# Kernel optimization log

Hardware: AMD Instinct MI355X
Metric: run time of the kernel (lower is better)

## Reference

```python
import jax, jax.numpy as jnp
import numpy as np

D_MODEL = 1024
NUM_HEADS = 16
D_K = D_MODEL // NUM_HEADS


def setup_inputs() -> dict:
    key = jax.random.key(0)
    ks = jax.random.split(key, 12)
    B, S = 2, 2048
    s = 1.0 / np.sqrt(D_MODEL)
    return {
        "Q": jax.random.normal(ks[0], (B, S, D_MODEL), jnp.float32),
        "K": jax.random.normal(ks[1], (B, S, D_MODEL), jnp.float32),
        "V": jax.random.normal(ks[2], (B, S, D_MODEL), jnp.float32),
        "Wq": jax.random.normal(ks[3], (D_MODEL, D_MODEL), jnp.float32) * s,
        "bq": jax.random.normal(ks[4], (D_MODEL,), jnp.float32) * s,
        "Wk": jax.random.normal(ks[5], (D_MODEL, D_MODEL), jnp.float32) * s,
        "bk": jax.random.normal(ks[6], (D_MODEL,), jnp.float32) * s,
        "Wv": jax.random.normal(ks[7], (D_MODEL, D_MODEL), jnp.float32) * s,
        "bv": jax.random.normal(ks[8], (D_MODEL,), jnp.float32) * s,
        "Wfc": jax.random.normal(ks[9], (D_MODEL, D_MODEL), jnp.float32) * s,
        "bfc": jax.random.normal(ks[10], (D_MODEL,), jnp.float32) * s,
    }


def reference(Q, K, V, Wq, bq, Wk, bk, Wv, bv, Wfc, bfc):
    B, S, _ = Q.shape
    # Linear projections, then split heads: [B, S, D] -> [B, H, S, d_k]
    def split_heads(x):
        return x.reshape(B, S, NUM_HEADS, D_K).transpose(0, 2, 1, 3)
    q = split_heads(Q @ Wq + bq)
    k = split_heads(K @ Wk + bk)
    v = split_heads(V @ Wv + bv)
    # Scaled dot-product attention (mask=None path)
    scores = jnp.einsum('bhqd,bhkd->bhqk', q, k) / jnp.sqrt(jnp.asarray(D_K, q.dtype))
    attention = jax.nn.softmax(scores, axis=-1)  # [B, H, S, S]
    context = jnp.einsum('bhqk,bhkd->bhqd', attention, v)
    context = context.transpose(0, 2, 1, 3).reshape(B, S, D_MODEL)
    output = context @ Wfc + bfc
    return output, attention
```

## Files before the change

### kernel.cpp

```cpp
#include <hip/hip_runtime.h>
#include <hip/hip_bf16.h>
#include <stdint.h>


typedef __bf16 bf16_t;
typedef __bf16 bf16x8 __attribute__((ext_vector_type(8)));
typedef float  f32x4  __attribute__((ext_vector_type(4)));

#define MFMA16(a, b, c) __builtin_amdgcn_mfma_f32_16x16x32_bf16((a), (b), (c), 0, 0, 0)

__global__ __launch_bounds__(256)
void wtrans_kernel(const float* w0, const float* w1, const float* w2,
                   const float* w3, bf16_t* wt)
{
  const float* W = blockIdx.z == 0 ? w0 : blockIdx.z == 1 ? w1
                 : blockIdx.z == 2 ? w2 : w3;
  bf16_t* O = wt + ((size_t)blockIdx.z << 20);
  __shared__ bf16_t tile[64][72];
  const int t = threadIdx.x;
  const int r0 = blockIdx.y * 64, c0 = blockIdx.x * 64;
  {
    const int r = t >> 2, cg = (t & 3) * 16;
    const float4* src = (const float4*)(W + (size_t)(r0 + r) * 1024 + c0 + cg);
#pragma unroll
    for (int u = 0; u < 4; ++u) {
      float4 f = src[u];
      tile[r][cg + u * 4 + 0] = (bf16_t)f.x;
      tile[r][cg + u * 4 + 1] = (bf16_t)f.y;
      tile[r][cg + u * 4 + 2] = (bf16_t)f.z;
      tile[r][cg + u * 4 + 3] = (bf16_t)f.w;
    }
  }
  __syncthreads();
  {
    const int c = t >> 2, rg = (t & 3) * 16;
    bf16x8 v0, v1;
#pragma unroll
    for (int u = 0; u < 8; ++u) { v0[u] = tile[rg + u][c]; v1[u] = tile[rg + 8 + u][c]; }
    bf16x8* dst = (bf16x8*)(O + (size_t)(c0 + c) * 1024 + r0 + rg);
    dst[0] = v0; dst[1] = v1;
  }
}

__global__ __launch_bounds__(256)
void vtrans_kernel(const bf16_t* vb, bf16_t* vT)
{
  __shared__ bf16_t tile[64][72];
  const int t = threadIdx.x;
  const int bh = blockIdx.y;
  const int s0 = blockIdx.x * 64;
  {
    const int s = t >> 2, dg = (t & 3) * 16;
    const bf16x8* src = (const bf16x8*)(vb + ((size_t)bh * 2048 + s0 + s) * 64 + dg);
    bf16x8 a = src[0], b = src[1];
#pragma unroll
    for (int u = 0; u < 8; ++u) { tile[s][dg + u] = a[u]; tile[s][dg + 8 + u] = b[u]; }
  }
  __syncthreads();
  {
    const int d = t >> 2, sg = (t & 3) * 16;
    bf16x8 v0, v1;
#pragma unroll
    for (int u = 0; u < 8; ++u) { v0[u] = tile[sg + u][d]; v1[u] = tile[sg + 8 + u][d]; }
    bf16x8* dst = (bf16x8*)(vT + ((size_t)bh * 64 + d) * 2048 + s0 + sg);
    dst[0] = v0; dst[1] = v1;
  }
}

template<bool A_BF16, bool OUT_SPLIT>
__global__ __launch_bounds__(256, 2)
void gemm_kernel(const void* A0, const void* A1, const void* A2,
                 const bf16_t* WTbase,
                 const float* b0, const float* b1, const float* b2,
                 void* Obase, size_t ostride)
{
  const int z = blockIdx.z;
  const void*  Aptr = z == 0 ? A0 : z == 1 ? A1 : A2;
  const float* bias = z == 0 ? b0 : z == 1 ? b1 : b2;
  const bf16_t* WT  = WTbase + ((size_t)z << 20);

  __shared__ bf16_t As[128 * 32];
  __shared__ bf16_t Bs[128 * 32];

  const int tid = threadIdx.x;
  const int lane = tid & 63, wv = tid >> 6;
  const int quad = lane >> 4, lr = lane & 15;
  const int wm = wv >> 1, wn = wv & 1;
  const int lin2 = blockIdx.y * 8 + blockIdx.x;
  const int idx  = lin2 >> 3;
  const int m0 = (((lin2 & 7) << 2) + (idx >> 3)) * 128;
  const int n0 = (idx & 7) * 128;

  f32x4 acc[4][4];
#pragma unroll
  for (int i = 0; i < 4; ++i)
#pragma unroll
    for (int j = 0; j < 4; ++j) acc[i][j] = (f32x4){0.f, 0.f, 0.f, 0.f};

  const int srow = tid >> 1;
  const int shalf = tid & 1;
  const int swz = (srow >> 1) & 3;
  bf16_t* as0 = &As[srow * 32 + (((shalf * 2)    ) ^ swz) * 8];
  bf16_t* as1 = &As[srow * 32 + (((shalf * 2) + 1) ^ swz) * 8];
  bf16_t* bs0 = &Bs[srow * 32 + (((shalf * 2)    ) ^ swz) * 8];
  bf16_t* bs1 = &Bs[srow * 32 + (((shalf * 2) + 1) ^ swz) * 8];

  for (int kt = 0; kt < 1024; kt += 32) {
    bf16x8 av0, av1, bv0, bv1;
    if (A_BF16) {
      const bf16x8* p = (const bf16x8*)((const bf16_t*)Aptr +
                          (size_t)(m0 + srow) * 1024 + kt + shalf * 16);
      av0 = p[0]; av1 = p[1];
    } else {
      const float4* p = (const float4*)((const float*)Aptr +
                          (size_t)(m0 + srow) * 1024 + kt + shalf * 16);
      float4 f0 = p[0], f1 = p[1], f2 = p[2], f3 = p[3];
      av0[0]=(bf16_t)f0.x; av0[1]=(bf16_t)f0.y; av0[2]=(bf16_t)f0.z; av0[3]=(bf16_t)f0.w;
      av0[4]=(bf16_t)f1.x; av0[5]=(bf16_t)f1.y; av0[6]=(bf16_t)f1.z; av0[7]=(bf16_t)f1.w;
      av1[0]=(bf16_t)f2.x; av1[1]=(bf16_t)f2.y; av1[2]=(bf16_t)f2.z; av1[3]=(bf16_t)f2.w;
      av1[4]=(bf16_t)f3.x; av1[5]=(bf16_t)f3.y; av1[6]=(bf16_t)f3.z; av1[7]=(bf16_t)f3.w;
    }
    {
      const bf16x8* p = (const bf16x8*)(WT + (size_t)(n0 + srow) * 1024 + kt + shalf * 16);
      bv0 = p[0]; bv1 = p[1];
    }
    __syncthreads();
    *(bf16x8*)as0 = av0; *(bf16x8*)as1 = av1;
    *(bf16x8*)bs0 = bv0; *(bf16x8*)bs1 = bv1;
    __syncthreads();
    bf16x8 af[4], bfr[4];
#pragma unroll
    for (int i = 0; i < 4; ++i) {
      const int row = wm * 64 + i * 16 + lr;
      af[i] = *(bf16x8*)&As[row * 32 + (quad ^ ((row >> 1) & 3)) * 8];
      const int nn = wn * 64 + i * 16 + lr;
      bfr[i] = *(bf16x8*)&Bs[nn * 32 + (quad ^ ((nn >> 1) & 3)) * 8];
    }
#pragma unroll
    for (int i = 0; i < 4; ++i)
#pragma unroll
      for (int j = 0; j < 4; ++j)
        acc[i][j] = MFMA16(af[i], bfr[j], acc[i][j]);
  }

  if (OUT_SPLIT) {
    bf16_t* O = (bf16_t*)Obase + (size_t)z * ostride;
#pragma unroll
    for (int i = 0; i < 4; ++i) {
      const int mbase = m0 + wm * 64 + i * 16 + quad * 4;
#pragma unroll
      for (int j = 0; j < 4; ++j) {
        const int n = n0 + wn * 64 + j * 16 + lr;
        const float bv = bias[n];
        const int h = n >> 6, d = n & 63;
#pragma unroll
        for (int r = 0; r < 4; ++r) {
          const int m = mbase + r;
          const int b = m >> 11, s = m & 2047;
          O[((size_t)(b * 16 + h) * 2048 + s) * 64 + d] = (bf16_t)(acc[i][j][r] + bv);
        }
      }
    }
  } else {
    float* O = (float*)Obase;
#pragma unroll
    for (int i = 0; i < 4; ++i) {
      const int mbase = m0 + wm * 64 + i * 16 + quad * 4;
#pragma unroll
      for (int j = 0; j < 4; ++j) {
        const int n = n0 + wn * 64 + j * 16 + lr;
        const float bv = bias[n];
#pragma unroll
        for (int r = 0; r < 4; ++r)
          O[(size_t)(mbase + r) * 1024 + n] = acc[i][j][r] + bv;
      }
    }
  }
}

__global__ __launch_bounds__(256, 2)
void attn_kernel(const bf16_t* qb, const bf16_t* kb, const bf16_t* vT,
                 float* attn, bf16_t* ctx)
{
  __shared__ bf16_t P[16 * 2048];
  __shared__ float wpart[4][16];
  __shared__ float inv16[16];
  const int tid = threadIdx.x;
  const int lane = tid & 63, wv = tid >> 6;
  const int quad = lane >> 4, lr = lane & 15;
  const int lin  = blockIdx.y * 128 + blockIdx.x;
  const int virt = ((lin & 7) << 9) + (lin >> 3);
  const int bh   = virt >> 7;
  const int row0 = (virt & 127) * 16;

  const bf16x8* qp = (const bf16x8*)(qb + ((size_t)bh * 2048 + row0 + lr) * 64 + quad * 8);
  const bf16x8 a0 = qp[0];
  const bf16x8 a1 = qp[4];

  float sums[4] = {0.f, 0.f, 0.f, 0.f};

  for (int ct = 0; ct < 32; ++ct) {
    const int n0 = wv * 512 + ct * 16;
    const bf16x8* kp = (const bf16x8*)(kb + ((size_t)bh * 2048 + n0 + lr) * 64 + quad * 8);
    const bf16x8 b0v = kp[0];
    const bf16x8 b1v = kp[4];
    f32x4 sacc = {0.f, 0.f, 0.f, 0.f};
    sacc = MFMA16(a0, b0v, sacc);
    sacc = MFMA16(a1, b1v, sacc);
#pragma unroll
    for (int r = 0; r < 4; ++r) {
      const float p = __expf(sacc[r] * 0.125f);
      const bf16_t pb = (bf16_t)p;
      sums[r] += (float)pb;
      const int prow = quad * 4 + r;
      P[prow * 2048 + ((n0 + lr) ^ ((prow & 7) << 3))] = pb;
    }
  }
#pragma unroll
  for (int m = 1; m < 16; m <<= 1) {
#pragma unroll
    for (int r = 0; r < 4; ++r) sums[r] += __shfl_xor(sums[r], m, 64);
  }
  if (lr == 0) {
#pragma unroll
    for (int r = 0; r < 4; ++r) wpart[wv][quad * 4 + r] = sums[r];
  }
  __syncthreads();
  if (tid < 16)
    inv16[tid] = 1.0f / (wpart[0][tid] + wpart[1][tid] + wpart[2][tid] + wpart[3][tid]);
  __syncthreads();

  {
    float* abase = attn + ((size_t)bh * 2048 + row0) * 2048 + tid * 8;
    for (int r = 0; r < 16; ++r) {
      const float inv = inv16[r];
      const bf16x8 pv = *(const bf16x8*)&P[r * 2048 + ((tid * 8) ^ ((r & 7) << 3))];
      f32x4 o0, o1;
      o0[0] = (float)pv[0] * inv; o0[1] = (float)pv[1] * inv;
      o0[2] = (float)pv[2] * inv; o0[3] = (float)pv[3] * inv;
      o1[0] = (float)pv[4] * inv; o1[1] = (float)pv[5] * inv;
      o1[2] = (float)pv[6] * inv; o1[3] = (float)pv[7] * inv;
      f32x4* dst = (f32x4*)(abase + (size_t)r * 2048);
      __builtin_nontemporal_store(o0, dst);
      __builtin_nontemporal_store(o1, dst + 1);
    }
  }

  {
    f32x4 cacc = {0.f, 0.f, 0.f, 0.f};
    const bf16_t* vbase = vT + ((size_t)bh * 64 + wv * 16 + lr) * 2048;
    for (int kt = 0; kt < 64; ++kt) {
      const bf16x8 af  = *(const bf16x8*)&P[lr * 2048 + ((kt * 32 + quad * 8) ^ ((lr & 7) << 3))];
      const bf16x8 bfv = *(const bf16x8*)(vbase + kt * 32 + quad * 8);
      cacc = MFMA16(af, bfv, cacc);
    }
    const int b = bh >> 4, h = bh & 15;
#pragma unroll
    for (int r = 0; r < 4; ++r) {
      const int row = quad * 4 + r;
      ctx[(size_t)(b * 2048 + row0 + row) * 1024 + h * 64 + wv * 16 + lr] =
          (bf16_t)(cacc[r] * inv16[row]);
    }
  }
}

extern "C" void kernel_launch(void* const* d_in, const int* in_sizes, int n_in,
                              void* d_out, int out_size, void* d_ws, size_t ws_size,
                              hipStream_t stream)
{
  const float* Q   = (const float*)d_in[0];
  const float* K   = (const float*)d_in[1];
  const float* V   = (const float*)d_in[2];
  const float* Wq  = (const float*)d_in[3];
  const float* bq  = (const float*)d_in[4];
  const float* Wk  = (const float*)d_in[5];
  const float* bk  = (const float*)d_in[6];
  const float* Wv  = (const float*)d_in[7];
  const float* bv  = (const float*)d_in[8];
  const float* Wfc = (const float*)d_in[9];
  const float* bfc = (const float*)d_in[10];

  char* ws = (char*)d_ws;
  bf16_t* wt   = (bf16_t*)ws;
  bf16_t* qb   = (bf16_t*)(ws + (size_t)8  * (1 << 20));
  bf16_t* kb   = (bf16_t*)(ws + (size_t)16 * (1 << 20));
  bf16_t* vb   = (bf16_t*)(ws + (size_t)24 * (1 << 20));
  bf16_t* vT   = (bf16_t*)(ws + (size_t)32 * (1 << 20));
  bf16_t* ctx  = (bf16_t*)(ws + (size_t)40 * (1 << 20));

  float* out  = (float*)d_out;
  float* attn = out + (size_t)4194304;

  dim3 blk(256);
  wtrans_kernel<<<dim3(16, 16, 4), blk, 0, stream>>>(Wq, Wk, Wv, Wfc, wt);
  gemm_kernel<false, true><<<dim3(8, 32, 3), blk, 0, stream>>>(
      Q, K, V, wt, bq, bk, bv, qb, (size_t)4194304);
  vtrans_kernel<<<dim3(32, 32), blk, 0, stream>>>(vb, vT);
  attn_kernel<<<dim3(128, 32), blk, 0, stream>>>(qb, kb, vT, attn, ctx);
  gemm_kernel<true, false><<<dim3(8, 32, 1), blk, 0, stream>>>(
      ctx, ctx, ctx, wt + ((size_t)3 << 20), bfc, bfc, bfc, out, 0);
}
```

Baseline: 884.5 us.

## Double-buffer GEMM with direct global-to-LDS loads and fuse V transpose into projection

Rewrites the projection GEMM main loop to use a 64-wide K tile with double-buffered LDS. The weight tile (and the A tile when it is already bf16) is fetched with global_load_lds, so the load for the next tile overlaps the MFMAs on the current one and the loop has one barrier per step. The V projection now writes its output directly in transposed [b,h,d,s] layout, which removes the separate vtrans kernel and its round trip through memory. LDS use grows to 64KB per block, which may reduce occupancy at the requested 2 blocks per CU.

After: 907.3 us. +2.6%, slower.

```diff
diff --git a/kernel.cpp b/kernel.cpp
--- a/kernel.cpp
+++ b/kernel.cpp
@@ -5,9 +5,14 @@
 
 typedef __bf16 bf16_t;
 typedef __bf16 bf16x8 __attribute__((ext_vector_type(8)));
+typedef __bf16 bf16x4 __attribute__((ext_vector_type(4)));
 typedef float  f32x4  __attribute__((ext_vector_type(4)));
 
 #define MFMA16(a, b, c) __builtin_amdgcn_mfma_f32_16x16x32_bf16((a), (b), (c), 0, 0, 0)
+
+#define GLDS(g, l) __builtin_amdgcn_global_load_lds( \
+    (const __attribute__((address_space(1))) void*)(g), \
+    (__attribute__((address_space(3))) void*)(l), 16, 0, 0)
 
 __global__ __launch_bounds__(256)
 void wtrans_kernel(const float* w0, const float* w1, const float* w2,
@@ -42,45 +47,20 @@
   }
 }
 
-__global__ __launch_bounds__(256)
-void vtrans_kernel(const bf16_t* vb, bf16_t* vT)
-{
-  __shared__ bf16_t tile[64][72];
-  const int t = threadIdx.x;
-  const int bh = blockIdx.y;
-  const int s0 = blockIdx.x * 64;
-  {
-    const int s = t >> 2, dg = (t & 3) * 16;
-    const bf16x8* src = (const bf16x8*)(vb + ((size_t)bh * 2048 + s0 + s) * 64 + dg);
-    bf16x8 a = src[0], b = src[1];
-#pragma unroll
-    for (int u = 0; u < 8; ++u) { tile[s][dg + u] = a[u]; tile[s][dg + 8 + u] = b[u]; }
-  }
-  __syncthreads();
-  {
-    const int d = t >> 2, sg = (t & 3) * 16;
-    bf16x8 v0, v1;
-#pragma unroll
-    for (int u = 0; u < 8; ++u) { v0[u] = tile[sg + u][d]; v1[u] = tile[sg + 8 + u][d]; }
-    bf16x8* dst = (bf16x8*)(vT + ((size_t)bh * 64 + d) * 2048 + s0 + sg);
-    dst[0] = v0; dst[1] = v1;
-  }
-}
-
 template<bool A_BF16, bool OUT_SPLIT>
 __global__ __launch_bounds__(256, 2)
 void gemm_kernel(const void* A0, const void* A1, const void* A2,
                  const bf16_t* WTbase,
                  const float* b0, const float* b1, const float* b2,
-                 void* Obase, size_t ostride)
+                 void* Obase, size_t ostride, bf16_t* vTout)
 {
   const int z = blockIdx.z;
   const void*  Aptr = z == 0 ? A0 : z == 1 ? A1 : A2;
   const float* bias = z == 0 ? b0 : z == 1 ? b1 : b2;
   const bf16_t* WT  = WTbase + ((size_t)z << 20);
 
-  __shared__ bf16_t As[128 * 32];
-  __shared__ bf16_t Bs[128 * 32];
+  __shared__ bf16_t As[2][128 * 64];
+  __shared__ bf16_t Bs[2][128 * 64];
 
   const int tid = threadIdx.x;
   const int lane = tid & 63, wv = tid >> 6;
@@ -97,67 +77,137 @@
 #pragma unroll
     for (int j = 0; j < 4; ++j) acc[i][j] = (f32x4){0.f, 0.f, 0.f, 0.f};
 
-  const int srow = tid >> 1;
-  const int shalf = tid & 1;
-  const int swz = (srow >> 1) & 3;
-  bf16_t* as0 = &As[srow * 32 + (((shalf * 2)    ) ^ swz) * 8];
-  bf16_t* as1 = &As[srow * 32 + (((shalf * 2) + 1) ^ swz) * 8];
-  bf16_t* bs0 = &Bs[srow * 32 + (((shalf * 2)    ) ^ swz) * 8];
-  bf16_t* bs1 = &Bs[srow * 32 + (((shalf * 2) + 1) ^ swz) * 8];
-
-  for (int kt = 0; kt < 1024; kt += 32) {
-    bf16x8 av0, av1, bv0, bv1;
+  const int gr = wv * 8 + (lane >> 3);
+  const int gc = ((lane & 7) ^ (lane >> 3)) << 3;
+  const bf16_t* bsrc = WT + (size_t)(n0 + gr) * 1024 + gc;
+  const bf16_t* absrc = (const bf16_t*)Aptr + (size_t)(m0 + gr) * 1024 + gc;
+
+  const int ar_ = tid >> 1, ah_ = tid & 1;
+  const float* afsrc = (const float*)Aptr + (size_t)(m0 + ar_) * 1024 + ah_ * 32;
+  int awofs[4];
+#pragma unroll
+  for (int c = 0; c < 4; ++c)
+    awofs[c] = ar_ * 64 + ((((ah_ << 2) + c) ^ (ar_ & 7)) << 3);
+
+  int arow[4], brow[4];
+#pragma unroll
+  for (int i = 0; i < 4; ++i) {
+    arow[i] = (wm * 64 + i * 16 + lr) * 64;
+    brow[i] = (wn * 64 + i * 16 + lr) * 64;
+  }
+  const int ach0 = ((quad)     ^ (lr & 7)) << 3;
+  const int ach1 = ((4 + quad) ^ (lr & 7)) << 3;
+
+  {
     if (A_BF16) {
-      const bf16x8* p = (const bf16x8*)((const bf16_t*)Aptr +
-                          (size_t)(m0 + srow) * 1024 + kt + shalf * 16);
-      av0 = p[0]; av1 = p[1];
+#pragma unroll
+      for (int n = 0; n < 4; ++n)
+        GLDS(absrc + n * 32768, &As[0][(n * 32 + wv * 8) * 64]);
     } else {
-      const float4* p = (const float4*)((const float*)Aptr +
-                          (size_t)(m0 + srow) * 1024 + kt + shalf * 16);
-      float4 f0 = p[0], f1 = p[1], f2 = p[2], f3 = p[3];
-      av0[0]=(bf16_t)f0.x; av0[1]=(bf16_t)f0.y; av0[2]=(bf16_t)f0.z; av0[3]=(bf16_t)f0.w;
-      av0[4]=(bf16_t)f1.x; av0[5]=(bf16_t)f1.y; av0[6]=(bf16_t)f1.z; av0[7]=(bf16_t)f1.w;
-      av1[0]=(bf16_t)f2.x; av1[1]=(bf16_t)f2.y; av1[2]=(bf16_t)f2.z; av1[3]=(bf16_t)f2.w;
-      av1[4]=(bf16_t)f3.x; av1[5]=(bf16_t)f3.y; av1[6]=(bf16_t)f3.z; av1[7]=(bf16_t)f3.w;
-    }
-    {
-      const bf16x8* p = (const bf16x8*)(WT + (size_t)(n0 + srow) * 1024 + kt + shalf * 16);
-      bv0 = p[0]; bv1 = p[1];
+      const float4* p = (const float4*)afsrc;
+      float4 areg[8];
+#pragma unroll
+      for (int u = 0; u < 8; ++u) areg[u] = p[u];
+#pragma unroll
+      for (int n = 0; n < 4; ++n)
+        GLDS(bsrc + n * 32768, &Bs[0][(n * 32 + wv * 8) * 64]);
+#pragma unroll
+      for (int c = 0; c < 4; ++c) {
+        const float4 f0 = areg[2 * c], f1 = areg[2 * c + 1];
+        bf16x8 v;
+        v[0]=(bf16_t)f0.x; v[1]=(bf16_t)f0.y; v[2]=(bf16_t)f0.z; v[3]=(bf16_t)f0.w;
+        v[4]=(bf16_t)f1.x; v[5]=(bf16_t)f1.y; v[6]=(bf16_t)f1.z; v[7]=(bf16_t)f1.w;
+        *(bf16x8*)&As[0][awofs[c]] = v;
+      }
+    }
+    if (A_BF16) {
+#pragma unroll
+      for (int n = 0; n < 4; ++n)
+        GLDS(bsrc + n * 32768, &Bs[0][(n * 32 + wv * 8) * 64]);
     }
     __syncthreads();
-    *(bf16x8*)as0 = av0; *(bf16x8*)as1 = av1;
-    *(bf16x8*)bs0 = bv0; *(bf16x8*)bs1 = bv1;
-    __syncthreads();
-    bf16x8 af[4], bfr[4];
-#pragma unroll
-    for (int i = 0; i < 4; ++i) {
-      const int row = wm * 64 + i * 16 + lr;
-      af[i] = *(bf16x8*)&As[row * 32 + (quad ^ ((row >> 1) & 3)) * 8];
-      const int nn = wn * 64 + i * 16 + lr;
-      bfr[i] = *(bf16x8*)&Bs[nn * 32 + (quad ^ ((nn >> 1) & 3)) * 8];
-    }
-#pragma unroll
-    for (int i = 0; i < 4; ++i)
-#pragma unroll
-      for (int j = 0; j < 4; ++j)
-        acc[i][j] = MFMA16(af[i], bfr[j], acc[i][j]);
+  }
+
+  for (int t = 0; t < 16; ++t) {
+    const int cur = t & 1, nxt = cur ^ 1;
+    const int ktn = t * 64 + 64;
+    float4 areg[8];
+    if (t < 15) {
+      if (A_BF16) {
+#pragma unroll
+        for (int n = 0; n < 4; ++n)
+          GLDS(absrc + n * 32768 + ktn, &As[nxt][(n * 32 + wv * 8) * 64]);
+      } else {
+        const float4* p = (const float4*)(afsrc + ktn);
+#pragma unroll
+        for (int u = 0; u < 8; ++u) areg[u] = p[u];
+      }
+#pragma unroll
+      for (int n = 0; n < 4; ++n)
+        GLDS(bsrc + n * 32768 + ktn, &Bs[nxt][(n * 32 + wv * 8) * 64]);
+    }
+#pragma unroll
+    for (int h = 0; h < 2; ++h) {
+      const int ach = h ? ach1 : ach0;
+      bf16x8 af[4], bfv[4];
+#pragma unroll
+      for (int i = 0; i < 4; ++i) af[i]  = *(const bf16x8*)&As[cur][arow[i] + ach];
+#pragma unroll
+      for (int j = 0; j < 4; ++j) bfv[j] = *(const bf16x8*)&Bs[cur][brow[j] + ach];
+#pragma unroll
+      for (int i = 0; i < 4; ++i)
+#pragma unroll
+        for (int j = 0; j < 4; ++j)
+          acc[i][j] = MFMA16(af[i], bfv[j], acc[i][j]);
+    }
+    if (t < 15) {
+      if (!A_BF16) {
+#pragma unroll
+        for (int c = 0; c < 4; ++c) {
+          const float4 f0 = areg[2 * c], f1 = areg[2 * c + 1];
+          bf16x8 v;
+          v[0]=(bf16_t)f0.x; v[1]=(bf16_t)f0.y; v[2]=(bf16_t)f0.z; v[3]=(bf16_t)f0.w;
+          v[4]=(bf16_t)f1.x; v[5]=(bf16_t)f1.y; v[6]=(bf16_t)f1.z; v[7]=(bf16_t)f1.w;
+          *(bf16x8*)&As[nxt][awofs[c]] = v;
+        }
+      }
+      __syncthreads();
+    }
   }
 
   if (OUT_SPLIT) {
-    bf16_t* O = (bf16_t*)Obase + (size_t)z * ostride;
-#pragma unroll
-    for (int i = 0; i < 4; ++i) {
-      const int mbase = m0 + wm * 64 + i * 16 + quad * 4;
-#pragma unroll
-      for (int j = 0; j < 4; ++j) {
-        const int n = n0 + wn * 64 + j * 16 + lr;
-        const float bv = bias[n];
-        const int h = n >> 6, d = n & 63;
-#pragma unroll
-        for (int r = 0; r < 4; ++r) {
-          const int m = mbase + r;
-          const int b = m >> 11, s = m & 2047;
-          O[((size_t)(b * 16 + h) * 2048 + s) * 64 + d] = (bf16_t)(acc[i][j][r] + bv);
+    if (z == 2) {
+#pragma unroll
+      for (int i = 0; i < 4; ++i) {
+        const int mbase = m0 + wm * 64 + i * 16 + quad * 4;
+        const int bb = mbase >> 11, s0 = mbase & 2047;
+#pragma unroll
+        for (int j = 0; j < 4; ++j) {
+          const int n = n0 + wn * 64 + j * 16 + lr;
+          const float bv = bias[n];
+          const int h = n >> 6, d = n & 63;
+          bf16x4 vv;
+#pragma unroll
+          for (int r = 0; r < 4; ++r) vv[r] = (bf16_t)(acc[i][j][r] + bv);
+          *(bf16x4*)&vTout[((size_t)((bb * 16 + h) * 64 + d)) * 2048 + s0] = vv;
+        }
+      }
+    } else {
+      bf16_t* O = (bf16_t*)Obase + (size_t)z * ostride;
+#pragma unroll
+      for (int i = 0; i < 4; ++i) {
+        const int mbase = m0 + wm * 64 + i * 16 + quad * 4;
+#pragma unroll
+        for (int j = 0; j < 4; ++j) {
+          const int n = n0 + wn * 64 + j * 16 + lr;
+          const float bv = bias[n];
+          const int h = n >> 6, d = n & 63;
+#pragma unroll
+          for (int r = 0; r < 4; ++r) {
+            const int m = mbase + r;
+            const int b = m >> 11, s = m & 2047;
+            O[((size_t)(b * 16 + h) * 2048 + s) * 64 + d] = (bf16_t)(acc[i][j][r] + bv);
+          }
         }
       }
     }
@@ -284,7 +334,6 @@
   bf16_t* wt   = (bf16_t*)ws;
   bf16_t* qb   = (bf16_t*)(ws + (size_t)8  * (1 << 20));
   bf16_t* kb   = (bf16_t*)(ws + (size_t)16 * (1 << 20));
-  bf16_t* vb   = (bf16_t*)(ws + (size_t)24 * (1 << 20));
   bf16_t* vT   = (bf16_t*)(ws + (size_t)32 * (1 << 20));
   bf16_t* ctx  = (bf16_t*)(ws + (size_t)40 * (1 << 20));
 
@@ -294,9 +343,8 @@
   dim3 blk(256);
   wtrans_kernel<<<dim3(16, 16, 4), blk, 0, stream>>>(Wq, Wk, Wv, Wfc, wt);
   gemm_kernel<false, true><<<dim3(8, 32, 3), blk, 0, stream>>>(
-      Q, K, V, wt, bq, bk, bv, qb, (size_t)4194304);
-  vtrans_kernel<<<dim3(32, 32), blk, 0, stream>>>(vb, vT);
+      Q, K, V, wt, bq, bk, bv, qb, (size_t)4194304, vT);
   attn_kernel<<<dim3(128, 32), blk, 0, stream>>>(qb, kb, vT, attn, ctx);
   gemm_kernel<true, false><<<dim3(8, 32, 1), blk, 0, stream>>>(
-      ctx, ctx, ctx, wt + ((size_t)3 << 20), bfc, bfc, bfc, out, 0);
+      ctx, ctx, ctx, wt + ((size_t)3 << 20), bfc, bfc, bfc, out, 0, nullptr);
 }
```
